# Performance work log

Measured on AMD Instinct MI355X. Metric: run time of the kernel, lower is better.

## Reference

```python
import jax, jax.numpy as jnp
import numpy as np

B, P, K, G_PER, F_IN, H, NECK = 16, 512, 32, 8, 59, 128, 512
N = B * P
E = N * K
G = N // G_PER
EPS = 1e-5


def setup_inputs() -> dict:
    rng = np.random.default_rng(0)
    f32 = lambda a: jnp.asarray(a, jnp.float32)
    x = f32(rng.standard_normal((N, F_IN)))
    pos = f32(rng.standard_normal((N, 3)) * 8.0)
    nrm = rng.standard_normal((N, 3))
    normal = f32(nrm / np.linalg.norm(nrm, axis=1, keepdims=True))
    # synthetic radius-graph edges: K neighbors per node within its own graph, incl. self edge
    nbr = rng.integers(0, P, size=(N, K))
    nbr[:, 0] = np.arange(N) % P  # self edge guarantees every dst segment is non-empty
    starts = np.repeat(np.arange(B) * P, P)
    src = jnp.asarray((starts[:, None] + nbr).reshape(-1), jnp.int32)
    dst = jnp.asarray(np.repeat(np.arange(N), K), jnp.int32)
    # raw (unnormalized but consecutive-run) residue labels, relabeled inside reference
    pool_batch = jnp.asarray(np.repeat(np.arange(G) * 3 + 7, G_PER), jnp.int32)
    mask_t = f32(np.repeat(rng.integers(0, 2, size=G), G_PER))
    def lin(i, o, bias=True):
        w = f32(rng.standard_normal((i, o)) / np.sqrt(i))
        return (w, f32(np.zeros(o))) if bias else w
    lin_w, lin_b = lin(F_IN, H)
    src_w = lin(F_IN, H, bias=False)
    dst_w = lin(F_IN, H, bias=False)
    posnn_w, posnn_b = lin(6, H)
    attnn_w, attnn_b = lin(H, H)
    neck_w, neck_b = lin(H, NECK)
    mlp1_w, mlp1_b = lin(NECK, 256)
    mlp2_w, mlp2_b = lin(256, 1)
    gb = lambda n: (f32(1.0 + 0.1 * rng.standard_normal(n)), f32(0.1 * rng.standard_normal(n)))
    posnn_g, posnn_bb = gb(H)
    attnn_g, attnn_bb = gb(H)
    neck_g, neck_bb = gb(NECK)
    mlp1_g, mlp1_bb = gb(256)
    return dict(x=x, pos=pos, normal=normal, mask_t=mask_t, pool_batch=pool_batch,
                src=src, dst=dst, lin_w=lin_w, lin_b=lin_b, src_w=src_w, dst_w=dst_w,
                posnn_w=posnn_w, posnn_b=posnn_b, posnn_g=posnn_g, posnn_bb=posnn_bb,
                attnn_w=attnn_w, attnn_b=attnn_b, attnn_g=attnn_g, attnn_bb=attnn_bb,
                neck_w=neck_w, neck_b=neck_b, neck_g=neck_g, neck_bb=neck_bb,
                mlp1_w=mlp1_w, mlp1_b=mlp1_b, mlp1_g=mlp1_g, mlp1_bb=mlp1_bb,
                mlp2_w=mlp2_w, mlp2_b=mlp2_b)


def bn_relu(h, g, b):
    # eval-mode BatchNorm1d (running_mean=0, running_var=1) + ReLU; Dropout is identity in eval
    return jax.nn.relu(h * (g / jnp.sqrt(1.0 + EPS)) + b)


def reference(x, pos, normal, mask_t, pool_batch, src, dst,
              lin_w, lin_b, src_w, dst_w,
              posnn_w, posnn_b, posnn_g, posnn_bb,
              attnn_w, attnn_b, attnn_g, attnn_bb,
              neck_w, neck_b, neck_g, neck_bb,
              mlp1_w, mlp1_b, mlp1_g, mlp1_bb,
              mlp2_w, mlp2_b):
    n = x.shape[0]
    # vectorized form of the per-element relabel loop: consecutive runs -> 0..G-1
    chg = jnp.concatenate([jnp.zeros((1,), jnp.int32),
                           (pool_batch[1:] != pool_batch[:-1]).astype(jnp.int32)])
    pb = jnp.cumsum(chg)
    # --- PointTransformerConv (gather -> pos_nn/attn_nn MLPs -> segment softmax -> scatter-add)
    v = x @ lin_w + lin_b                      # value projection [N,H]
    a_src = (x @ src_w)[src]                   # lin_src(x_j)   [E,H]
    a_dst = (x @ dst_w)[dst]                   # lin_dst(x_i)   [E,H]
    rel = jnp.concatenate([pos[dst] - pos[src], normal[dst] - normal[src]], axis=-1)  # [E,6]
    delta = bn_relu(rel @ posnn_w + posnn_b, posnn_g, posnn_bb)                       # [E,H]
    alpha = bn_relu((a_dst - a_src + delta) @ attnn_w + attnn_b, attnn_g, attnn_bb)   # [E,H]
    amax = jax.ops.segment_max(alpha, dst, num_segments=n)
    e = jnp.exp(alpha - amax[dst])
    den = jax.ops.segment_sum(e, dst, num_segments=n)
    attn = e / (den[dst] + 1e-16)              # per-destination softmax over neighbors
    h = jax.ops.segment_sum(attn * (v[src] + delta), dst, num_segments=n)  # [N,H]
    # --- neck, residue max-pool, head
    h = bn_relu(h @ neck_w + neck_b, neck_g, neck_bb)          # [N,512]
    gfeat = jax.ops.segment_max(h, pb, num_segments=G)         # global_max_pool  [G,512]
    gfeat = bn_relu(gfeat @ mlp1_w + mlp1_b, mlp1_g, mlp1_bb)  # [G,256]
    out = gfeat @ mlp2_w + mlp2_b                              # [G,1]
    mask_g = jax.ops.segment_max(mask_t, pb, num_segments=G)   # pooled mask_t
    # original does out[mask_t]; we zero non-selected rows to keep shapes static
    return out * (mask_g == 1.0).astype(out.dtype)[:, None]
```

## Files before the change

kernel.cpp:

```cpp
#include <hip/hip_runtime.h>
#include <hip/hip_bf16.h>
#include <cmath>

#define N_NODES 8192
#define F_INPUT 59
#define H 128
#define K 32
#define NECK 512
#define GPER 8
#define NG 1024
#define EPS_BN 1e-5f
#define DPITCH 136
#define XPITCH 72
#define PLANE 272

typedef short bf16x8 __attribute__((ext_vector_type(8)));
typedef float f32x16 __attribute__((ext_vector_type(16)));

__device__ __forceinline__ void split_bf(float v, short& hi, short& lo) {
    unsigned u = __float_as_uint(v);
    float hif = __uint_as_float(u & 0xffff0000u);
    hi = (short)(u >> 16);
    lo = (short)(__float_as_uint(v - hif) >> 16);
}
__device__ __forceinline__ short f2bfrn(float f) {
    __hip_bfloat16 b = __float2bfloat16(f);
    return *reinterpret_cast<short*>(&b);
}

__device__ __forceinline__ int bfrag_idx(int k, int c, int k16) {
    int ct = c >> 5, ln = c & 31;
    int s = k >> 4, hf = (k >> 3) & 1, kk = k & 7;
    return ((((ct * k16 + s) * 2 + hf) * 32 + ln) * 8 + kk);
}

__global__ __launch_bounds__(256) void prep_kernel(
    const float* __restrict__ lin_w,
    const float* __restrict__ src_w, const float* __restrict__ dst_w,
    const float* __restrict__ posnn_w,
    const float* __restrict__ attnn_w, const float* __restrict__ attnn_g,
    const float* __restrict__ neck_w,
    short* __restrict__ w3hi, short* __restrict__ w3lo,
    short* __restrict__ pwhi, short* __restrict__ pwlo,
    short* __restrict__ awhi, short* __restrict__ awlo,
    short* __restrict__ nwhi, short* __restrict__ nwlo)
{
    const int b = blockIdx.x;
    if (b < F_INPUT) {
        const int c = threadIdx.x;
        if (c < H) {
            float a1 = 0.f, a2 = 0.f;
            for (int k = 0; k < H; k++) {
                float wa = attnn_w[k * H + c];
                a1 = fmaf(src_w[b * H + k], wa, a1);
                a2 = fmaf(dst_w[b * H + k], wa, a2);
            }
            short hi, lo; int idx;
            split_bf(lin_w[b * H + c], hi, lo);
            idx = bfrag_idx(b, c, 4);       w3hi[idx] = hi; w3lo[idx] = lo;
            split_bf(a1, hi, lo);
            idx = bfrag_idx(b, 128 + c, 4); w3hi[idx] = hi; w3lo[idx] = lo;
            split_bf(a2, hi, lo);
            idx = bfrag_idx(b, 256 + c, 4); w3hi[idx] = hi; w3lo[idx] = lo;
        }
    } else if (b == F_INPUT) {
        for (int t = threadIdx.x; t < 5 * 384; t += 256) {
            int k = F_INPUT + t / 384, c = t % 384;
            int idx = bfrag_idx(k, c, 4);
            w3hi[idx] = 0; w3lo[idx] = 0;
        }
    } else if (b == F_INPUT + 1) {
        for (int idx = threadIdx.x; idx < 2048; idx += 256) {
            int kk = idx & 7; int t = idx >> 3;
            int l2 = t & 31; t >>= 5;
            int hb = t & 1;  t >>= 1;
            int ct = t;
            int k = hb * 8 + kk, c = ct * 32 + l2;
            float wv = (k < 6) ? posnn_w[k * H + c] : 0.f;
            short hi, lo; split_bf(wv, hi, lo);
            pwhi[idx] = hi; pwlo[idx] = lo;
        }
    } else if (b < F_INPUT + 2 + 64) {
        int idx = (b - F_INPUT - 2) * 256 + threadIdx.x;
        int kk = idx & 7; int t = idx >> 3;
        int l2 = t & 31; t >>= 5;
        int hb = t & 1;  t >>= 1;
        int s  = t & 7;  t >>= 3;
        int c = t * 32 + l2, k = s * 16 + hb * 8 + kk;
        float scale = attnn_g[c] * rsqrtf(1.f + EPS_BN);
        short hi, lo; split_bf(attnn_w[k * H + c] * scale, hi, lo);
        awhi[idx] = hi; awlo[idx] = lo;
    } else {
        int idx = (b - F_INPUT - 2 - 64) * 256 + threadIdx.x;
        int kk = idx & 7; int t = idx >> 3;
        int l2 = t & 31; t >>= 5;
        int hb = t & 1;  t >>= 1;
        int s  = t & 7;  t >>= 3;
        int c = t * 32 + l2, k = s * 16 + hb * 8 + kk;
        short hi, lo; split_bf(neck_w[k * NECK + c], hi, lo);
        nwhi[idx] = hi; nwlo[idx] = lo;
    }
}

__global__ __launch_bounds__(256) void proj_kernel(
    const float* __restrict__ x, const float* __restrict__ lin_b,
    const float* __restrict__ attnn_g, const float* __restrict__ attnn_b,
    const float* __restrict__ attnn_bb,
    const short* __restrict__ w3hi, const short* __restrict__ w3lo,
    float2* __restrict__ vx, float* __restrict__ xdb)
{
    const int n0 = blockIdx.x * 32;
    const int tid = threadIdx.x;
    const int wave = tid >> 6;
    const int lane = tid & 63;
    const int hf = lane >> 5;
    const int ln = lane & 31;

    __shared__ __align__(16) short xhi[32][XPITCH];
    __shared__ __align__(16) short xlo[32][XPITCH];

    for (int idx = tid; idx < 32 * F_INPUT; idx += 256) {
        int n = idx / F_INPUT, k = idx - n * F_INPUT;
        short hi, lo; split_bf(x[n0 * F_INPUT + idx], hi, lo);
        xhi[n][k] = hi; xlo[n][k] = lo;
    }
    if (tid < 32 * 5) {
        int n = tid / 5, k = F_INPUT + tid % 5;
        xhi[n][k] = 0; xlo[n][k] = 0;
    }
    __syncthreads();

    f32x16 acc[3];
    #pragma unroll
    for (int t = 0; t < 3; t++)
        #pragma unroll
        for (int r = 0; r < 16; r++) acc[t][r] = 0.f;

    #pragma unroll
    for (int s = 0; s < 4; s++) {
        bf16x8 ah = *(const bf16x8*)&xhi[ln][s * 16 + hf * 8];
        bf16x8 al = *(const bf16x8*)&xlo[ln][s * 16 + hf * 8];
        #pragma unroll
        for (int t = 0; t < 3; t++) {
            const int ct = wave + 4 * t;
            const int boff = (((ct * 4 + s) * 2 + hf) * 32 + ln) * 8;
            bf16x8 bh = *(const bf16x8*)&w3hi[boff];
            bf16x8 bl = *(const bf16x8*)&w3lo[boff];
            acc[t] = __builtin_amdgcn_mfma_f32_32x32x16_bf16(ah, bl, acc[t], 0, 0, 0);
            acc[t] = __builtin_amdgcn_mfma_f32_32x32x16_bf16(al, bh, acc[t], 0, 0, 0);
            acc[t] = __builtin_amdgcn_mfma_f32_32x32x16_bf16(ah, bh, acc[t], 0, 0, 0);
        }
    }
    const int c = wave * 32 + ln;
    const float lb  = lin_b[c];
    const float as_ = attnn_g[c] * rsqrtf(1.f + EPS_BN);
    const float cbn = fmaf(attnn_b[c], as_, attnn_bb[c]);
    #pragma unroll
    for (int r = 0; r < 16; r++) {
        int node = n0 + (r & 3) + 8 * (r >> 2) + 4 * hf;
        vx[node * H + c] = make_float2(as_ * acc[1][r], acc[0][r] + lb);
        xdb[node * H + c] = fmaf(acc[2][r], as_, cbn);
    }
}

__global__ __launch_bounds__(256) void edge_kernel(
    const float* __restrict__ pos, const float* __restrict__ normal,
    const int* __restrict__ src,
    const float2* __restrict__ vx, const float* __restrict__ xdb,
    const float* __restrict__ posnn_b, const float* __restrict__ posnn_g,
    const float* __restrict__ posnn_bb,
    const short* __restrict__ pwhi, const short* __restrict__ pwlo,
    const short* __restrict__ awhi, const short* __restrict__ awlo,
    unsigned* __restrict__ h2)
{
    const int i0 = blockIdx.x * 2;
    const int tid = threadIdx.x;
    const int wave = tid >> 6;
    const int lane = tid & 63;
    const int hf = lane >> 5;
    const int ln = lane & 31;

    __shared__ int srcs[2][K];
    __shared__ __align__(16) short relh[4 * PLANE];
    __shared__ __align__(16) short rell[4 * PLANE];
    __shared__ __align__(16) short dpk[32 * PLANE];

    if (tid < 64) {
        int n = tid >> 5, jj = tid & 31;
        int i = i0 + n;
        int s = src[i * K + jj];
        srcs[n][jj] = s;
        short h_, l_;
        const int b0 = (n * 2) * PLANE + jj * 8;
        const int b1 = (n * 2 + 1) * PLANE + jj * 8;
        #pragma unroll
        for (int k = 0; k < 3; k++) {
            split_bf(pos[i * 3 + k] - pos[s * 3 + k], h_, l_);
            relh[b0 + k] = h_; rell[b0 + k] = l_;
            split_bf(normal[i * 3 + k] - normal[s * 3 + k], h_, l_);
            relh[b0 + k + 3] = h_; rell[b0 + k + 3] = l_;
        }
        #pragma unroll
        for (int k = 6; k < 8; k++) { relh[b0 + k] = 0; rell[b0 + k] = 0; }
        #pragma unroll
        for (int k = 0; k < 8; k++) { relh[b1 + k] = 0; rell[b1 + k] = 0; }
    }

    const int cc = wave * 32 + ln;
    const float ps  = posnn_g[cc] * rsqrtf(1.f + EPS_BN);
    const float pbn = fmaf(posnn_b[cc], ps, posnn_bb[cc]);

    const bf16x8 pbh = *(const bf16x8*)&pwhi[((wave * 2 + hf) * 32 + ln) * 8];
    const bf16x8 pbl = *(const bf16x8*)&pwlo[((wave * 2 + hf) * 32 + ln) * 8];

    const int dbase = ((cc >> 4) * 2 + ((cc >> 3) & 1)) * PLANE + (cc & 7);

    __syncthreads();

    float dreg[2][16];
    #pragma unroll
    for (int n = 0; n < 2; n++) {
        bf16x8 ah = *(const bf16x8*)&relh[(n * 2 + hf) * PLANE + ln * 8];
        bf16x8 al = *(const bf16x8*)&rell[(n * 2 + hf) * PLANE + ln * 8];
        f32x16 da;
        #pragma unroll
        for (int r = 0; r < 16; r++) da[r] = 0.f;
        da = __builtin_amdgcn_mfma_f32_32x32x16_bf16(ah, pbl, da, 0, 0, 0);
        da = __builtin_amdgcn_mfma_f32_32x32x16_bf16(al, pbh, da, 0, 0, 0);
        da = __builtin_amdgcn_mfma_f32_32x32x16_bf16(ah, pbh, da, 0, 0, 0);
        #pragma unroll
        for (int r = 0; r < 16; r++) {
            int j = (r & 3) + 8 * (r >> 2) + 4 * hf;
            float d = fmaxf(fmaf(da[r], ps, pbn), 0.f);
            dreg[n][r] = d;
            dpk[n * 16 * PLANE + dbase + j * 8] = f2bfrn(d);
        }
    }
    __syncthreads();

    const short* whb = awhi + wave * 8 * 2 * 32 * 8;
    const short* wlb = awlo + wave * 8 * 2 * 32 * 8;

    #pragma unroll
    for (int n = 0; n < 2; n++) {
        const int i = i0 + n;
        f32x16 acc;
        #pragma unroll
        for (int r = 0; r < 16; r++) acc[r] = 0.f;
        #pragma unroll
        for (int s = 0; s < 8; s++) {
            bf16x8 ah = *(const bf16x8*)&dpk[((n * 8 + s) * 2 + hf) * PLANE + ln * 8];
            const int boff = ((s * 2 + hf) * 32 + ln) * 8;
            bf16x8 bh = *(const bf16x8*)&whb[boff];
            bf16x8 bl = *(const bf16x8*)&wlb[boff];
            acc = __builtin_amdgcn_mfma_f32_32x32x16_bf16(ah, bh, acc, 0, 0, 0);
            acc = __builtin_amdgcn_mfma_f32_32x32x16_bf16(ah, bl, acc, 0, 0, 0);
        }

        const float base = xdb[i * H + cc];
        float a[16], vv[16];
        float m = 0.f;
        #pragma unroll
        for (int r = 0; r < 16; r++) {
            int j = (r & 3) + 8 * (r >> 2) + 4 * hf;
            float2 g = vx[srcs[n][j] * H + cc];
            float av = fmaxf(acc[r] + base - g.x, 0.f);
            a[r] = av; vv[r] = g.y;
            m = fmaxf(m, av);
        }
        m = fmaxf(m, __shfl_xor(m, 32, 64));
        float den = 0.f;
        #pragma unroll
        for (int r = 0; r < 16; r++) {
            float e = __expf(a[r] - m);
            a[r] = e; den += e;
        }
        den += __shfl_xor(den, 32, 64);
        const float inv = 1.f / (den + 1e-16f);

        float hsum = 0.f;
        #pragma unroll
        for (int r = 0; r < 16; r++)
            hsum = fmaf(a[r], vv[r] + dreg[n][r], hsum);
        hsum += __shfl_xor(hsum, 32, 64);
        hsum *= inv;
        if (hf == 0) {
            unsigned u = __float_as_uint(hsum);
            unsigned hib = u & 0xffff0000u;
            unsigned lo = __float_as_uint(hsum - __uint_as_float(hib)) >> 16;
            h2[i * H + cc] = (lo << 16) | (u >> 16);
        }
    }
}

__global__ __launch_bounds__(256) void neck_head_kernel(
    const unsigned* __restrict__ h2,
    const short* __restrict__ nwhi, const short* __restrict__ nwlo,
    const float* __restrict__ neck_b, const float* __restrict__ neck_g,
    const float* __restrict__ neck_bb,
    const float* __restrict__ mask_t,
    const float* __restrict__ mlp1_w, const float* __restrict__ mlp1_b,
    const float* __restrict__ mlp1_g, const float* __restrict__ mlp1_bb,
    const float* __restrict__ mlp2_w, const float* __restrict__ mlp2_b,
    float* __restrict__ out)
{
    const int blk = blockIdx.x;
    const int n0 = blk * 32;
    const int tid = threadIdx.x;
    const int wave = tid >> 6;
    const int lane = tid & 63;
    const int hf = lane >> 5;
    const int ln = lane & 31;

    __shared__ __align__(16) short a_hi[32][DPITCH];
    __shared__ __align__(16) short a_lo[32][DPITCH];
    __shared__ float gfeat_l[4][NECK];
    __shared__ float red_l[4][4][256];

    for (int d = tid; d < 32 * H; d += 256) {
        unsigned u = h2[(n0 + (d >> 7)) * H + (d & 127)];
        a_hi[d >> 7][d & 127] = (short)(u & 0xffffu);
        a_lo[d >> 7][d & 127] = (short)(u >> 16);
    }
    __syncthreads();

    f32x16 acc[4];
    #pragma unroll
    for (int t = 0; t < 4; t++)
        #pragma unroll
        for (int r = 0; r < 16; r++) acc[t][r] = 0.f;

    #pragma unroll
    for (int s = 0; s < 8; s++) {
        bf16x8 ah = *(const bf16x8*)&a_hi[ln][s * 16 + hf * 8];
        bf16x8 al = *(const bf16x8*)&a_lo[ln][s * 16 + hf * 8];
        #pragma unroll
        for (int t = 0; t < 4; t++) {
            const int ct = wave * 4 + t;
            const int boff = (((ct * 8 + s) * 2 + hf) * 32 + ln) * 8;
            bf16x8 bh = *(const bf16x8*)&nwhi[boff];
            bf16x8 bl = *(const bf16x8*)&nwlo[boff];
            acc[t] = __builtin_amdgcn_mfma_f32_32x32x16_bf16(ah, bl, acc[t], 0, 0, 0);
            acc[t] = __builtin_amdgcn_mfma_f32_32x32x16_bf16(al, bh, acc[t], 0, 0, 0);
            acc[t] = __builtin_amdgcn_mfma_f32_32x32x16_bf16(ah, bh, acc[t], 0, 0, 0);
        }
    }

    #pragma unroll
    for (int t = 0; t < 4; t++) {
        const int c = wave * 128 + t * 32 + ln;
        const float s  = neck_g[c] * rsqrtf(1.f + EPS_BN);
        const float bnb = fmaf(neck_b[c], s, neck_bb[c]);
        #pragma unroll
        for (int g = 0; g < 4; g++) {
            float m = 0.f;
            #pragma unroll
            for (int q = 0; q < 4; q++)
                m = fmaxf(m, fmaf(acc[t][4 * g + q], s, bnb));
            m = fmaxf(m, __shfl_xor(m, 32, 64));
            if (hf == 0) gfeat_l[g][c] = m;
        }
    }
    __syncthreads();

    const int c4 = lane;
    float ph[4][4];
    #pragma unroll
    for (int g = 0; g < 4; g++)
        #pragma unroll
        for (int mm = 0; mm < 4; mm++) ph[g][mm] = 0.f;

    const int k0 = wave * 128;
    for (int k = 0; k < 128; k += 4) {
        float4 gv[4];
        #pragma unroll
        for (int g = 0; g < 4; g++) gv[g] = *(const float4*)&gfeat_l[g][k0 + k];
        #pragma unroll
        for (int kk = 0; kk < 4; kk++) {
            float w0 = mlp1_w[(k0 + k + kk) * 256 + c4];
            float w1 = mlp1_w[(k0 + k + kk) * 256 + c4 + 64];
            float w2 = mlp1_w[(k0 + k + kk) * 256 + c4 + 128];
            float w3 = mlp1_w[(k0 + k + kk) * 256 + c4 + 192];
            #pragma unroll
            for (int g = 0; g < 4; g++) {
                float gvk = (&gv[g].x)[kk];
                ph[g][0] = fmaf(gvk, w0, ph[g][0]);
                ph[g][1] = fmaf(gvk, w1, ph[g][1]);
                ph[g][2] = fmaf(gvk, w2, ph[g][2]);
                ph[g][3] = fmaf(gvk, w3, ph[g][3]);
            }
        }
    }
    #pragma unroll
    for (int g = 0; g < 4; g++)
        #pragma unroll
        for (int mm = 0; mm < 4; mm++)
            red_l[wave][g][c4 + 64 * mm] = ph[g][mm];
    __syncthreads();

    {
        const int g = wave;
        float part = 0.f;
        #pragma unroll
        for (int mm = 0; mm < 4; mm++) {
            const int c = c4 + 64 * mm;
            float sum = mlp1_b[c] + red_l[0][g][c] + red_l[1][g][c]
                      + red_l[2][g][c] + red_l[3][g][c];
            float s = mlp1_g[c] * rsqrtf(1.f + EPS_BN);
            float val = fmaxf(fmaf(sum, s, mlp1_bb[c]), 0.f);
            part = fmaf(val, mlp2_w[c], part);
        }
        #pragma unroll
        for (int off = 32; off > 0; off >>= 1) part += __shfl_xor(part, off, 64);
        if (lane == 0) {
            const int gg = blk * 4 + g;
            float mm = mask_t[gg * GPER];
            #pragma unroll
            for (int n = 1; n < GPER; n++) mm = fmaxf(mm, mask_t[gg * GPER + n]);
            out[gg] = (mm == 1.0f) ? (part + mlp2_b[0]) : 0.f;
        }
    }
}

extern "C" void kernel_launch(void* const* d_in, const int* in_sizes, int n_in,
                              void* d_out, int out_size, void* d_ws, size_t ws_size,
                              hipStream_t stream)
{
    const float* x        = (const float*)d_in[0];
    const float* pos      = (const float*)d_in[1];
    const float* normal   = (const float*)d_in[2];
    const float* mask_t   = (const float*)d_in[3];
    const int*   src      = (const int*)d_in[5];
    const float* lin_w    = (const float*)d_in[7];
    const float* lin_b    = (const float*)d_in[8];
    const float* src_w    = (const float*)d_in[9];
    const float* dst_w    = (const float*)d_in[10];
    const float* posnn_w  = (const float*)d_in[11];
    const float* posnn_b  = (const float*)d_in[12];
    const float* posnn_g  = (const float*)d_in[13];
    const float* posnn_bb = (const float*)d_in[14];
    const float* attnn_w  = (const float*)d_in[15];
    const float* attnn_b  = (const float*)d_in[16];
    const float* attnn_g  = (const float*)d_in[17];
    const float* attnn_bb = (const float*)d_in[18];
    const float* neck_w   = (const float*)d_in[19];
    const float* neck_b   = (const float*)d_in[20];
    const float* neck_g   = (const float*)d_in[21];
    const float* neck_bb  = (const float*)d_in[22];
    const float* mlp1_w   = (const float*)d_in[23];
    const float* mlp1_b   = (const float*)d_in[24];
    const float* mlp1_g   = (const float*)d_in[25];
    const float* mlp1_bb  = (const float*)d_in[26];
    const float* mlp2_w   = (const float*)d_in[27];
    const float* mlp2_b   = (const float*)d_in[28];

    float* ws = (float*)d_ws;
    float2*   vx   = (float2*)ws;
    float*    xdb  = (float*)(vx + (size_t)N_NODES * H);
    unsigned* h2   = (unsigned*)(xdb + (size_t)N_NODES * H);
    short*    w3hi = (short*)(h2 + (size_t)N_NODES * H);
    short*    w3lo = w3hi + 24576;
    short*    pwhi = w3lo + 24576;
    short*    pwlo = pwhi + 2048;
    short*    awhi = pwlo + 2048;
    short*    awlo = awhi + H * H;
    short*    nwhi = awlo + H * H;
    short*    nwlo = nwhi + H * NECK;

    prep_kernel<<<F_INPUT + 2 + 64 + 256, 256, 0, stream>>>(
        lin_w, src_w, dst_w, posnn_w, attnn_w, attnn_g, neck_w,
        w3hi, w3lo, pwhi, pwlo, awhi, awlo, nwhi, nwlo);
    proj_kernel<<<N_NODES / 32, 256, 0, stream>>>(x, lin_b, attnn_g, attnn_b, attnn_bb,
                                                  w3hi, w3lo, vx, xdb);
    edge_kernel<<<N_NODES / 2, 256, 0, stream>>>(pos, normal, src, vx, xdb,
                                                 posnn_b, posnn_g, posnn_bb,
                                                 pwhi, pwlo, awhi, awlo, h2);
    neck_head_kernel<<<N_NODES / 32, 256, 0, stream>>>(
        h2, nwhi, nwlo, neck_b, neck_g, neck_bb, mask_t,
        mlp1_w, mlp1_b, mlp1_g, mlp1_bb, mlp2_w, mlp2_b, (float*)d_out);
}
```

Baseline: 202.8 us.

## Fold log2e into attention weights, drop softmax max, prefetch gathers early

Pre-scales the attention-MLP weights and BN bias by log2(e) so the softmax can use exp2 directly. It removes the per-destination max subtraction and its shuffle reduction. The gathered vx values and xdb base are now loaded before the MFMA work so their latency overlaps compute, and the source index is pre-multiplied by H. Dropping the max subtraction risks overflow if attention logits get large, and holding the prefetched values raises register pressure.

```diff
diff --git a/kernel.cpp b/kernel.cpp
--- a/kernel.cpp
+++ b/kernel.cpp
@@ -10,6 +10,7 @@
 #define GPER 8
 #define NG 1024
 #define EPS_BN 1e-5f
+#define LOG2E 1.44269504088896340736f
 #define DPITCH 136
 #define XPITCH 72
 #define PLANE 272
@@ -87,7 +88,7 @@
         int hb = t & 1;  t >>= 1;
         int s  = t & 7;  t >>= 3;
         int c = t * 32 + l2, k = s * 16 + hb * 8 + kk;
-        float scale = attnn_g[c] * rsqrtf(1.f + EPS_BN);
+        float scale = attnn_g[c] * rsqrtf(1.f + EPS_BN) * LOG2E;
         short hi, lo; split_bf(attnn_w[k * H + c] * scale, hi, lo);
         awhi[idx] = hi; awlo[idx] = lo;
     } else {
@@ -153,8 +154,9 @@
     }
     const int c = wave * 32 + ln;
     const float lb  = lin_b[c];
-    const float as_ = attnn_g[c] * rsqrtf(1.f + EPS_BN);
-    const float cbn = fmaf(attnn_b[c], as_, attnn_bb[c]);
+    const float s0  = attnn_g[c] * rsqrtf(1.f + EPS_BN);
+    const float as_ = s0 * LOG2E;
+    const float cbn = fmaf(attnn_b[c], s0, attnn_bb[c]) * LOG2E;
     #pragma unroll
     for (int r = 0; r < 16; r++) {
         int node = n0 + (r & 3) + 8 * (r >> 2) + 4 * hf;
@@ -189,7 +191,7 @@
         int n = tid >> 5, jj = tid & 31;
         int i = i0 + n;
         int s = src[i * K + jj];
-        srcs[n][jj] = s;
+        srcs[n][jj] = s * H;
         short h_, l_;
         const int b0 = (n * 2) * PLANE + jj * 8;
         const int b1 = (n * 2 + 1) * PLANE + jj * 8;
@@ -216,6 +218,18 @@
     const int dbase = ((cc >> 4) * 2 + ((cc >> 3) & 1)) * PLANE + (cc & 7);
 
     __syncthreads();
+
+    float2 gv[2][16];
+    float base_[2];
+    #pragma unroll
+    for (int n = 0; n < 2; n++) {
+        base_[n] = xdb[(i0 + n) * H + cc];
+        #pragma unroll
+        for (int r = 0; r < 16; r++) {
+            int j = (r & 3) + 8 * (r >> 2) + 4 * hf;
+            gv[n][r] = vx[srcs[n][j] + cc];
+        }
+    }
 
     float dreg[2][16];
     #pragma unroll
@@ -257,23 +271,15 @@
             acc = __builtin_amdgcn_mfma_f32_32x32x16_bf16(ah, bl, acc, 0, 0, 0);
         }
 
-        const float base = xdb[i * H + cc];
-        float a[16], vv[16];
-        float m = 0.f;
+        const float base = base_[n];
+        float e[16];
+        float den = 0.f;
         #pragma unroll
         for (int r = 0; r < 16; r++) {
-            int j = (r & 3) + 8 * (r >> 2) + 4 * hf;
-            float2 g = vx[srcs[n][j] * H + cc];
-            float av = fmaxf(acc[r] + base - g.x, 0.f);
-            a[r] = av; vv[r] = g.y;
-            m = fmaxf(m, av);
-        }
-        m = fmaxf(m, __shfl_xor(m, 32, 64));
-        float den = 0.f;
-        #pragma unroll
-        for (int r = 0; r < 16; r++) {
-            float e = __expf(a[r] - m);
-            a[r] = e; den += e;
+            float av = fmaxf(acc[r] + base - gv[n][r].x, 0.f);
+            float ev = exp2f(av);
+            e[r] = ev;
+            den += ev;
         }
         den += __shfl_xor(den, 32, 64);
         const float inv = 1.f / (den + 1e-16f);
@@ -281,7 +287,7 @@
         float hsum = 0.f;
         #pragma unroll
         for (int r = 0; r < 16; r++)
-            hsum = fmaf(a[r], vv[r] + dreg[n][r], hsum);
+            hsum = fmaf(e[r], gv[n][r].y + dreg[n][r], hsum);
         hsum += __shfl_xor(hsum, 32, 64);
         hsum *= inv;
         if (hf == 0) {
```

New measurement: 208.2 us. +2.7%, slower.
